# Kernel optimization log

Hardware: AMD Instinct MI355X
Metric: run time of the kernel (lower is better)

The kernel has to match this reference:

```python
import jax, jax.numpy as jnp
import numpy as np


def setup_inputs() -> dict:
    key = jax.random.key(0)
    k1, k2, k3, k4 = jax.random.split(key, 4)
    B, S, IN, OUT = 4, 2048, 4096, 4096
    x = jax.random.normal(k1, (B, S, IN), dtype=jnp.float32)
    # 4-bit signed range [-8, 7], stored widened (torch uses int8)
    weight_quantized = jax.random.randint(k2, (OUT, IN), -8, 8, dtype=jnp.int32)
    # per-output-row scale, positive and small (abs-max / 7 style)
    weight_scale = jax.random.uniform(k3, (OUT,), dtype=jnp.float32) * 0.01 + 1e-4
    bias = jax.random.normal(k4, (OUT,), dtype=jnp.float32) * 0.01
    return {"x": x, "weight_quantized": weight_quantized,
            "weight_scale": weight_scale, "bias": bias}


def reference(x, weight_quantized, weight_scale, bias):
    # dequantize: [OUT, IN] int -> fp32 scaled per output row
    w = weight_quantized.astype(jnp.float32) * weight_scale[:, None]
    # F.linear: x @ w.T + bias  -> [B, S, OUT]
    out = jnp.einsum('bsi,oi->bso', x, w) + bias
    return out
```

## Files before the change

kernel.cpp:

```cpp
#include <hip/hip_runtime.h>
#include <hip/hip_bf16.h>

typedef __bf16 bf16x4 __attribute__((ext_vector_type(4)));
typedef __bf16 bf16x8 __attribute__((ext_vector_type(8)));
typedef float  floatx4 __attribute__((ext_vector_type(4)));

#define AS1 __attribute__((address_space(1)))
#define AS3 __attribute__((address_space(3)))

#define BM2 256
#define BN2 256
#define BK2 64
#define HALF (128 * 64)
#define ABUF (2 * HALF)

#define BARRIER() asm volatile("s_barrier" ::: "memory")

__global__ __launch_bounds__(256)
void cvt_both8(const float* __restrict__ xin, const int* __restrict__ win,
               __bf16* __restrict__ xout, __bf16* __restrict__ wout,
               int nx8, int nw8)
{
    const int stride = gridDim.x * 256;
    const int total  = nx8 + nw8;
    for (int i = blockIdx.x * 256 + threadIdx.x; i < total; i += stride) {
        if (i < nx8) {
            const float4* p = reinterpret_cast<const float4*>(xin) + (size_t)i * 2;
            float4 a = p[0], b = p[1];
            bf16x8 h;
            h[0] = (__bf16)a.x; h[1] = (__bf16)a.y; h[2] = (__bf16)a.z; h[3] = (__bf16)a.w;
            h[4] = (__bf16)b.x; h[5] = (__bf16)b.y; h[6] = (__bf16)b.z; h[7] = (__bf16)b.w;
            reinterpret_cast<bf16x8*>(xout)[i] = h;
        } else {
            int j = i - nx8;
            const int4* p = reinterpret_cast<const int4*>(win) + (size_t)j * 2;
            int4 a = p[0], b = p[1];
            bf16x8 h;
            h[0] = (__bf16)(float)a.x; h[1] = (__bf16)(float)a.y;
            h[2] = (__bf16)(float)a.z; h[3] = (__bf16)(float)a.w;
            h[4] = (__bf16)(float)b.x; h[5] = (__bf16)(float)b.y;
            h[6] = (__bf16)(float)b.z; h[7] = (__bf16)(float)b.w;
            reinterpret_cast<bf16x8*>(wout)[j] = h;
        }
    }
}

template<int Q>
__device__ __forceinline__ void mfma16(floatx4 (&acc)[8][4],
                                       const bf16x8 (&af)[2][2],
                                       const bf16x8 (&bfr)[4][2])
{
#pragma unroll
    for (int h = 0; h < 2; ++h)
#pragma unroll
        for (int ii = 0; ii < 2; ++ii)
#pragma unroll
            for (int j = 0; j < 4; ++j)
                acc[2 * Q + ii][j] = __builtin_amdgcn_mfma_f32_16x16x32_bf16(
                    af[ii][h], bfr[j][h], acc[2 * Q + ii][j], 0, 0, 0);
}

__device__ __forceinline__ void read_afH(bf16x8 (&dst)[2][2], const __bf16* p,
                                         int rowBase, int lm, int kq, int sw)
{
#pragma unroll
    for (int ii = 0; ii < 2; ++ii)
#pragma unroll
        for (int h = 0; h < 2; ++h)
            dst[ii][h] = *reinterpret_cast<const bf16x8*>(
                &p[(rowBase + ii * 16 + lm) * 64 + ((kq + h * 4) ^ sw) * 8]);
}

__device__ __forceinline__ void read_bfH(bf16x8 (&dst)[4][2], const __bf16* p,
                                         int wnh, int lm, int kq, int sw)
{
#pragma unroll
    for (int j = 0; j < 4; ++j)
#pragma unroll
        for (int h = 0; h < 2; ++h)
            dst[j][h] = *reinterpret_cast<const bf16x8*>(
                &p[(wnh + j * 16 + lm) * 64 + ((kq + h * 4) ^ sw) * 8]);
}

__global__ __launch_bounds__(512)
void gemm_bf16_bt_8ph(const __bf16* __restrict__ A, const __bf16* __restrict__ B,
                      const float* __restrict__ scale, const float* __restrict__ bias,
                      float* __restrict__ Out, int M, int N, int K)
{
    __shared__ __bf16 sA[2 * ABUF];
    __shared__ __bf16 sB[2 * ABUF];

    const int tid  = threadIdx.x;
    const int wave = tid >> 6;
    const int lane = tid & 63;
    const int row0 = blockIdx.y * BM2;
    const int col0 = blockIdx.x * BN2;

    const int sRow = lane >> 3;
    const int gBlk = (lane & 7) ^ sRow;
    const size_t aBase = (size_t)(row0 + wave * 8 + sRow) * K + gBlk * 8;
    const size_t bBase = (size_t)(col0 + wave * 8 + sRow) * K + gBlk * 8;
    const int dOff = wave * 8 * 64;

#define STG_A(buf, h, sub, kt_) \
    __builtin_amdgcn_global_load_lds( \
        (const AS1 void*)(A + aBase + (size_t)((h) * 128 + (sub) * 64) * K + (size_t)(kt_) * BK2), \
        (AS3 void*)(sA + (buf) * ABUF + (h) * HALF + (sub) * 64 * 64 + dOff), 16, 0, 0)
#define STG_B(buf, h, sub, kt_) \
    __builtin_amdgcn_global_load_lds( \
        (const AS1 void*)(B + bBase + (size_t)((h) * 128 + (sub) * 64) * K + (size_t)(kt_) * BK2), \
        (AS3 void*)(sB + (buf) * ABUF + (h) * HALF + (sub) * 64 * 64 + dOff), 16, 0, 0)
#define STGH_A(buf, h, kt_) do { STG_A(buf, h, 0, kt_); STG_A(buf, h, 1, kt_); } while (0)
#define STGH_B(buf, h, kt_) do { STG_B(buf, h, 0, kt_); STG_B(buf, h, 1, kt_); } while (0)

    const int hA  = wave >> 2;
    const int hB  = (wave & 3) >> 1;
    const int wnh = (wave & 1) * 64;
    const int lm  = lane & 15;
    const int kq  = lane >> 4;
    const int sw  = lm & 7;

    const __bf16* aH[2] = { sA + hA * HALF, sA + ABUF + hA * HALF };
    const __bf16* bH[2] = { sB + hB * HALF, sB + ABUF + hB * HALF };

    floatx4 acc[8][4];
#pragma unroll
    for (int i = 0; i < 8; ++i)
#pragma unroll
        for (int j = 0; j < 4; ++j)
            acc[i][j] = (floatx4)0.0f;

    bf16x8 bfr[4][2];
    bf16x8 af[2][2];
    const int nt = K / BK2;

    STGH_B(0, 0, 0); STGH_B(0, 1, 0);
    STGH_A(0, 0, 0); STGH_A(0, 1, 0);
    STGH_B(1, 0, 1); STGH_B(1, 1, 1);
    asm volatile("s_waitcnt vmcnt(4)" ::: "memory");
    BARRIER();

#define PH(Q, c, DOB, STAGE, DOVM)                                             \
    do {                                                                       \
        if (DOB) read_bfH(bfr, bH[c], wnh, lm, kq, sw);                        \
        read_afH(af, aH[c], (Q) * 32, lm, kq, sw);                             \
        STAGE;                                                                 \
        BARRIER();                                                             \
        __builtin_amdgcn_sched_barrier(0);                                     \
        __builtin_amdgcn_s_setprio(1);                                         \
        mfma16<Q>(acc, af, bfr);                                               \
        __builtin_amdgcn_s_setprio(0);                                         \
        __builtin_amdgcn_sched_barrier(0);                                     \
        if (DOVM) asm volatile("s_waitcnt vmcnt(4)" ::: "memory");             \
        BARRIER();                                                             \
    } while (0)

    for (int it = 0; it < nt / 2; ++it) {
        const int kt = 2 * it;
        const int e1 = kt + 1;
        const int e2 = (kt + 2 < nt) ? kt + 2 : 0;
        const int e3 = (kt + 3 < nt) ? kt + 3 : 0;

        PH(0, 0, true,  STGH_A(1, 0, e1), false);
        PH(1, 0, false, STGH_A(1, 1, e1), false);
        PH(2, 0, false, STGH_B(0, 0, e2), false);
        PH(3, 0, false, STGH_B(0, 1, e2), true );
        PH(0, 1, true,  STGH_A(0, 0, e2), false);
        PH(1, 1, false, STGH_A(0, 1, e2), false);
        PH(2, 1, false, STGH_B(1, 0, e3), false);
        PH(3, 1, false, STGH_B(1, 1, e3), true );
    }
    asm volatile("s_waitcnt vmcnt(0)" ::: "memory");
#undef PH
#undef STGH_A
#undef STGH_B
#undef STG_A
#undef STG_B

    const int wm = hA * 128;
    const int wn = (wave & 3) * 64;
#pragma unroll
    for (int j = 0; j < 4; ++j) {
        int n = col0 + wn + j * 16 + lm;
        float sc = scale[n];
        float bi = bias[n];
#pragma unroll
        for (int i = 0; i < 8; ++i) {
#pragma unroll
            for (int r = 0; r < 4; ++r) {
                int m = row0 + wm + i * 16 + kq * 4 + r;
                Out[(size_t)m * N + n] = sc * acc[i][j][r] + bi;
            }
        }
    }
}

#define BM 128
#define BN 128

__global__ __launch_bounds__(256)
void fp4linear_gemm(const float* __restrict__ X, const int* __restrict__ W,
                    const float* __restrict__ scale, const float* __restrict__ bias,
                    float* __restrict__ Out, int M, int N, int K)
{
    __shared__ __bf16 sA[BM * 32];
    __shared__ __bf16 sB[BN * 32];

    const int tid  = threadIdx.x;
    const int row0 = blockIdx.y * BM;
    const int col0 = blockIdx.x * BN;
    const int wave = tid >> 6;
    const int lane = tid & 63;
    const int wm = (wave >> 1) * 64;
    const int wn = (wave & 1) * 64;
    const int lm = lane & 15;
    const int kq = lane >> 4;

    floatx4 acc[4][4];
#pragma unroll
    for (int i = 0; i < 4; ++i)
#pragma unroll
        for (int j = 0; j < 4; ++j)
            acc[i][j] = (floatx4)0.0f;

    for (int k0 = 0; k0 < K; k0 += 32) {
        float4 fa[4];
        int4   ib[4];
#pragma unroll
        for (int l = 0; l < 4; ++l) {
            int idx = tid + l * 256;
            int r = idx >> 3, c4 = idx & 7;
            fa[l] = *reinterpret_cast<const float4*>(
                        &X[(size_t)(row0 + r) * K + k0 + c4 * 4]);
        }
#pragma unroll
        for (int l = 0; l < 4; ++l) {
            int idx = tid + l * 256;
            int r = idx >> 3, c4 = idx & 7;
            ib[l] = *reinterpret_cast<const int4*>(
                        &W[(size_t)(col0 + r) * K + k0 + c4 * 4]);
        }
        __syncthreads();
#pragma unroll
        for (int l = 0; l < 4; ++l) {
            int idx = tid + l * 256;
            int r = idx >> 3, c4 = idx & 7;
            bf16x4 h;
            h[0] = (__bf16)fa[l].x; h[1] = (__bf16)fa[l].y;
            h[2] = (__bf16)fa[l].z; h[3] = (__bf16)fa[l].w;
            *reinterpret_cast<bf16x4*>(&sA[r * 32 + c4 * 4]) = h;
        }
#pragma unroll
        for (int l = 0; l < 4; ++l) {
            int idx = tid + l * 256;
            int r = idx >> 3, c4 = idx & 7;
            bf16x4 h;
            h[0] = (__bf16)(float)ib[l].x; h[1] = (__bf16)(float)ib[l].y;
            h[2] = (__bf16)(float)ib[l].z; h[3] = (__bf16)(float)ib[l].w;
            *reinterpret_cast<bf16x4*>(&sB[r * 32 + c4 * 4]) = h;
        }
        __syncthreads();

        bf16x8 af[4], bfr[4];
#pragma unroll
        for (int i = 0; i < 4; ++i)
            af[i] = *reinterpret_cast<const bf16x8*>(
                        &sA[(wm + i * 16 + lm) * 32 + kq * 8]);
#pragma unroll
        for (int j = 0; j < 4; ++j)
            bfr[j] = *reinterpret_cast<const bf16x8*>(
                        &sB[(wn + j * 16 + lm) * 32 + kq * 8]);
#pragma unroll
        for (int i = 0; i < 4; ++i)
#pragma unroll
            for (int j = 0; j < 4; ++j)
                acc[i][j] = __builtin_amdgcn_mfma_f32_16x16x32_bf16(
                                af[i], bfr[j], acc[i][j], 0, 0, 0);
    }

#pragma unroll
    for (int j = 0; j < 4; ++j) {
        int n = col0 + wn + j * 16 + lm;
        float sc = scale[n];
        float bi = bias[n];
#pragma unroll
        for (int i = 0; i < 4; ++i) {
#pragma unroll
            for (int r = 0; r < 4; ++r) {
                int m = row0 + wm + i * 16 + kq * 4 + r;
                Out[(size_t)m * N + n] = sc * acc[i][j][r] + bi;
            }
        }
    }
}

extern "C" void kernel_launch(void* const* d_in, const int* in_sizes, int n_in,
                              void* d_out, int out_size, void* d_ws, size_t ws_size,
                              hipStream_t stream) {
    const float* x     = (const float*)d_in[0];
    const int*   wq    = (const int*)d_in[1];
    const float* scale = (const float*)d_in[2];
    const float* bias  = (const float*)d_in[3];
    float* out = (float*)d_out;

    const int N = in_sizes[2];
    const int K = in_sizes[1] / N;
    const int M = in_sizes[0] / K;

    const size_t xElems = (size_t)M * K;
    const size_t wElems = (size_t)N * K;
    const size_t need   = (xElems + wElems) * sizeof(__bf16);

    const bool cvt_ok = (ws_size >= need) && (xElems % 8 == 0) && (wElems % 8 == 0);
    const int  nt     = K / BK2;
    const bool gemm_ok = (M % BM2 == 0) && (N % BN2 == 0) && (K % BK2 == 0) &&
                         (nt % 2 == 0) && (nt >= 4);

    if (cvt_ok && gemm_ok) {
        __bf16* xb = (__bf16*)d_ws;
        __bf16* wb = xb + xElems;
        int nx8 = (int)(xElems / 8);
        int nw8 = (int)(wElems / 8);
        int total = nx8 + nw8;
        int cvtBlocks = (total + 255) / 256;
        if (cvtBlocks > 2048) cvtBlocks = 2048;
        hipLaunchKernelGGL(cvt_both8, dim3(cvtBlocks), dim3(256), 0, stream,
                           x, wq, xb, wb, nx8, nw8);
        hipLaunchKernelGGL(gemm_bf16_bt_8ph, dim3(N / BN2, M / BM2), dim3(512),
                           0, stream, xb, wb, scale, bias, out, M, N, K);
        return;
    }

    hipLaunchKernelGGL(fp4linear_gemm, dim3(N / BN, M / BM), dim3(256), 0, stream,
                       x, wq, scale, bias, out, M, N, K);
}
```

Baseline: 508.5 us.

## Fuse fp32/int32-to-bf16 conversion into GEMM tile loading via register staging

Drops the separate conversion kernel that wrote bf16 copies of x and the weights to workspace. The GEMM now loads fp32 activations and int32 weights directly, converts them in registers and writes swizzled bf16 tiles to LDS, using a reworked phase pipeline that splits the B fragments into two halves. This removes the extra global write and re-read of the converted operands and one kernel launch. In exchange, each tile fetches twice the bytes from global memory, the operands are re-read and re-converted across the many output tiles, and the direct global-to-LDS async loads become register round-trips with more VGPR pressure.

After: 1.185 ms. 133% more time.

```diff
diff --git a/kernel.cpp b/kernel.cpp
--- a/kernel.cpp
+++ b/kernel.cpp
@@ -16,48 +16,25 @@
 
 #define BARRIER() asm volatile("s_barrier" ::: "memory")
 
-__global__ __launch_bounds__(256)
-void cvt_both8(const float* __restrict__ xin, const int* __restrict__ win,
-               __bf16* __restrict__ xout, __bf16* __restrict__ wout,
-               int nx8, int nw8)
-{
-    const int stride = gridDim.x * 256;
-    const int total  = nx8 + nw8;
-    for (int i = blockIdx.x * 256 + threadIdx.x; i < total; i += stride) {
-        if (i < nx8) {
-            const float4* p = reinterpret_cast<const float4*>(xin) + (size_t)i * 2;
-            float4 a = p[0], b = p[1];
-            bf16x8 h;
-            h[0] = (__bf16)a.x; h[1] = (__bf16)a.y; h[2] = (__bf16)a.z; h[3] = (__bf16)a.w;
-            h[4] = (__bf16)b.x; h[5] = (__bf16)b.y; h[6] = (__bf16)b.z; h[7] = (__bf16)b.w;
-            reinterpret_cast<bf16x8*>(xout)[i] = h;
-        } else {
-            int j = i - nx8;
-            const int4* p = reinterpret_cast<const int4*>(win) + (size_t)j * 2;
-            int4 a = p[0], b = p[1];
-            bf16x8 h;
-            h[0] = (__bf16)(float)a.x; h[1] = (__bf16)(float)a.y;
-            h[2] = (__bf16)(float)a.z; h[3] = (__bf16)(float)a.w;
-            h[4] = (__bf16)(float)b.x; h[5] = (__bf16)(float)b.y;
-            h[6] = (__bf16)(float)b.z; h[7] = (__bf16)(float)b.w;
-            reinterpret_cast<bf16x8*>(wout)[j] = h;
-        }
-    }
-}
-
 template<int Q>
-__device__ __forceinline__ void mfma16(floatx4 (&acc)[8][4],
-                                       const bf16x8 (&af)[2][2],
-                                       const bf16x8 (&bfr)[4][2])
+__device__ __forceinline__ void mfma16s(floatx4 (&acc)[8][4],
+                                        const bf16x8 (&af)[2][2],
+                                        const bf16x8 (&bfA)[2][2],
+                                        const bf16x8 (&bfB)[2][2])
 {
 #pragma unroll
     for (int h = 0; h < 2; ++h)
 #pragma unroll
-        for (int ii = 0; ii < 2; ++ii)
-#pragma unroll
-            for (int j = 0; j < 4; ++j)
+        for (int ii = 0; ii < 2; ++ii) {
+#pragma unroll
+            for (int j = 0; j < 2; ++j)
                 acc[2 * Q + ii][j] = __builtin_amdgcn_mfma_f32_16x16x32_bf16(
-                    af[ii][h], bfr[j][h], acc[2 * Q + ii][j], 0, 0, 0);
+                    af[ii][h], bfA[j][h], acc[2 * Q + ii][j], 0, 0, 0);
+#pragma unroll
+            for (int j = 0; j < 2; ++j)
+                acc[2 * Q + ii][2 + j] = __builtin_amdgcn_mfma_f32_16x16x32_bf16(
+                    af[ii][h], bfB[j][h], acc[2 * Q + ii][2 + j], 0, 0, 0);
+        }
 }
 
 __device__ __forceinline__ void read_afH(bf16x8 (&dst)[2][2], const __bf16* p,
@@ -68,24 +45,24 @@
 #pragma unroll
         for (int h = 0; h < 2; ++h)
             dst[ii][h] = *reinterpret_cast<const bf16x8*>(
-                &p[(rowBase + ii * 16 + lm) * 64 + ((kq + h * 4) ^ sw) * 8]);
-}
-
-__device__ __forceinline__ void read_bfH(bf16x8 (&dst)[4][2], const __bf16* p,
-                                         int wnh, int lm, int kq, int sw)
-{
-#pragma unroll
-    for (int j = 0; j < 4; ++j)
+                &p[(rowBase + ii * 16 + lm) * BK2 + ((kq + h * 4) ^ sw) * 8]);
+}
+
+__device__ __forceinline__ void read_bf2(bf16x8 (&dst)[2][2], const __bf16* p,
+                                         int rowBase, int lm, int kq, int sw)
+{
+#pragma unroll
+    for (int j = 0; j < 2; ++j)
 #pragma unroll
         for (int h = 0; h < 2; ++h)
             dst[j][h] = *reinterpret_cast<const bf16x8*>(
-                &p[(wnh + j * 16 + lm) * 64 + ((kq + h * 4) ^ sw) * 8]);
+                &p[(rowBase + j * 16 + lm) * BK2 + ((kq + h * 4) ^ sw) * 8]);
 }
 
 __global__ __launch_bounds__(512)
-void gemm_bf16_bt_8ph(const __bf16* __restrict__ A, const __bf16* __restrict__ B,
-                      const float* __restrict__ scale, const float* __restrict__ bias,
-                      float* __restrict__ Out, int M, int N, int K)
+void gemm_fused(const float* __restrict__ X, const int* __restrict__ W,
+                const float* __restrict__ scale, const float* __restrict__ bias,
+                float* __restrict__ Out, int M, int N, int K)
 {
     __shared__ __bf16 sA[2 * ABUF];
     __shared__ __bf16 sB[2 * ABUF];
@@ -96,22 +73,44 @@
     const int row0 = blockIdx.y * BM2;
     const int col0 = blockIdx.x * BN2;
 
-    const int sRow = lane >> 3;
-    const int gBlk = (lane & 7) ^ sRow;
-    const size_t aBase = (size_t)(row0 + wave * 8 + sRow) * K + gBlk * 8;
-    const size_t bBase = (size_t)(col0 + wave * 8 + sRow) * K + gBlk * 8;
-    const int dOff = wave * 8 * 64;
-
-#define STG_A(buf, h, sub, kt_) \
-    __builtin_amdgcn_global_load_lds( \
-        (const AS1 void*)(A + aBase + (size_t)((h) * 128 + (sub) * 64) * K + (size_t)(kt_) * BK2), \
-        (AS3 void*)(sA + (buf) * ABUF + (h) * HALF + (sub) * 64 * 64 + dOff), 16, 0, 0)
-#define STG_B(buf, h, sub, kt_) \
-    __builtin_amdgcn_global_load_lds( \
-        (const AS1 void*)(B + bBase + (size_t)((h) * 128 + (sub) * 64) * K + (size_t)(kt_) * BK2), \
-        (AS3 void*)(sB + (buf) * ABUF + (h) * HALF + (sub) * 64 * 64 + dOff), 16, 0, 0)
-#define STGH_A(buf, h, kt_) do { STG_A(buf, h, 0, kt_); STG_A(buf, h, 1, kt_); } while (0)
-#define STGH_B(buf, h, kt_) do { STG_B(buf, h, 0, kt_); STG_B(buf, h, 1, kt_); } while (0)
+    const float* Ab = X + (size_t)row0 * K;
+    const int*   Wb = W + (size_t)col0 * K;
+
+#define U_ROW(j) ((tid + (j) * 512) >> 4)
+#define U_CB(j)  ((tid + (j) * 512) & 15)
+
+#define LD_CHUNK(set, SRC, h, kt_)                                             \
+    do { _Pragma("unroll") for (int j = 0; j < 4; ++j) {                       \
+        set[j] = *reinterpret_cast<const int4*>(                               \
+            (SRC) + (size_t)((h) * 128 + U_ROW(j)) * K                         \
+                  + (size_t)(kt_) * 64 + U_CB(j) * 4);                         \
+    } } while (0)
+
+#define LDS_BYTE(j, base2)                                                     \
+    ((base2) + U_ROW(j) * 128 + (((U_CB(j) >> 1) ^ (U_ROW(j) & 7)) * 16)       \
+             + (U_CB(j) & 1) * 8)
+
+#define WR_CHUNK_A(set, buf, h)                                                \
+    do { _Pragma("unroll") for (int j = 0; j < 4; ++j) {                       \
+        bf16x4 hv;                                                             \
+        hv[0] = (__bf16)__int_as_float(set[j].x);                              \
+        hv[1] = (__bf16)__int_as_float(set[j].y);                              \
+        hv[2] = (__bf16)__int_as_float(set[j].z);                              \
+        hv[3] = (__bf16)__int_as_float(set[j].w);                              \
+        *reinterpret_cast<bf16x4*>((char*)sA +                                 \
+            LDS_BYTE(j, ((buf) * ABUF + (h) * HALF) * 2)) = hv;                \
+    } } while (0)
+
+#define WR_CHUNK_B(set, buf, h)                                                \
+    do { _Pragma("unroll") for (int j = 0; j < 4; ++j) {                       \
+        bf16x4 hv;                                                             \
+        hv[0] = (__bf16)(float)set[j].x;                                       \
+        hv[1] = (__bf16)(float)set[j].y;                                       \
+        hv[2] = (__bf16)(float)set[j].z;                                       \
+        hv[3] = (__bf16)(float)set[j].w;                                       \
+        *reinterpret_cast<bf16x4*>((char*)sB +                                 \
+            LDS_BYTE(j, ((buf) * ABUF + (h) * HALF) * 2)) = hv;                \
+    } } while (0)
 
     const int hA  = wave >> 2;
     const int hB  = (wave & 3) >> 1;
@@ -130,52 +129,64 @@
         for (int j = 0; j < 4; ++j)
             acc[i][j] = (floatx4)0.0f;
 
-    bf16x8 bfr[4][2];
-    bf16x8 af[2][2];
+    bf16x8 bfA[2][2], bfB[2][2], af[2][2];
+    int4 s0[4], s1[4];
     const int nt = K / BK2;
 
-    STGH_B(0, 0, 0); STGH_B(0, 1, 0);
-    STGH_A(0, 0, 0); STGH_A(0, 1, 0);
-    STGH_B(1, 0, 1); STGH_B(1, 1, 1);
-    asm volatile("s_waitcnt vmcnt(4)" ::: "memory");
+    LD_CHUNK(s0, Ab, 0, 0); WR_CHUNK_A(s0, 0, 0);
+    LD_CHUNK(s0, Ab, 1, 0); WR_CHUNK_A(s0, 0, 1);
+    LD_CHUNK(s0, Wb, 0, 0); WR_CHUNK_B(s0, 0, 0);
+    LD_CHUNK(s0, Wb, 1, 0); WR_CHUNK_B(s0, 0, 1);
+    LD_CHUNK(s0, Wb, 0, 1); WR_CHUNK_B(s0, 1, 0);
+    LD_CHUNK(s1, Wb, 1, 1);
+    asm volatile("s_waitcnt lgkmcnt(0)" ::: "memory");
     BARRIER();
-
-#define PH(Q, c, DOB, STAGE, DOVM)                                             \
+    read_bf2(bfA, bH[0], wnh, lm, kq, sw);
+
+#define PHASE(Q, c, HEADX, ISSUE, POSTX, WRX)                                  \
     do {                                                                       \
-        if (DOB) read_bfH(bfr, bH[c], wnh, lm, kq, sw);                        \
+        HEADX;                                                                 \
         read_afH(af, aH[c], (Q) * 32, lm, kq, sw);                             \
-        STAGE;                                                                 \
+        ISSUE;                                                                 \
         BARRIER();                                                             \
         __builtin_amdgcn_sched_barrier(0);                                     \
         __builtin_amdgcn_s_setprio(1);                                         \
-        mfma16<Q>(acc, af, bfr);                                               \
+        mfma16s<Q>(acc, af, bfA, bfB);                                         \
         __builtin_amdgcn_s_setprio(0);                                         \
         __builtin_amdgcn_sched_barrier(0);                                     \
-        if (DOVM) asm volatile("s_waitcnt vmcnt(4)" ::: "memory");             \
+        POSTX;                                                                 \
+        WRX;                                                                   \
+        asm volatile("s_waitcnt lgkmcnt(0)" ::: "memory");                     \
         BARRIER();                                                             \
     } while (0)
+
+#define TILE(c, e1, e2)                                                        \
+    PHASE(0, c, read_bf2(bfB, bH[c], wnh + 32, lm, kq, sw),                    \
+          LD_CHUNK(s0, Ab, 0, e1), (void)0, WR_CHUNK_B(s1, (c) ^ 1, 1));       \
+    PHASE(1, c, (void)0, LD_CHUNK(s1, Ab, 1, e1), (void)0,                     \
+          WR_CHUNK_A(s0, (c) ^ 1, 0));                                         \
+    PHASE(2, c, (void)0, LD_CHUNK(s0, Wb, 0, e2), (void)0,                     \
+          WR_CHUNK_A(s1, (c) ^ 1, 1));                                         \
+    PHASE(3, c, (void)0, LD_CHUNK(s1, Wb, 1, e2),                              \
+          read_bf2(bfA, bH[(c) ^ 1], wnh, lm, kq, sw), WR_CHUNK_B(s0, (c), 0));
 
     for (int it = 0; it < nt / 2; ++it) {
         const int kt = 2 * it;
         const int e1 = kt + 1;
         const int e2 = (kt + 2 < nt) ? kt + 2 : 0;
-        const int e3 = (kt + 3 < nt) ? kt + 3 : 0;
-
-        PH(0, 0, true,  STGH_A(1, 0, e1), false);
-        PH(1, 0, false, STGH_A(1, 1, e1), false);
-        PH(2, 0, false, STGH_B(0, 0, e2), false);
-        PH(3, 0, false, STGH_B(0, 1, e2), true );
-        PH(0, 1, true,  STGH_A(0, 0, e2), false);
-        PH(1, 1, false, STGH_A(0, 1, e2), false);
-        PH(2, 1, false, STGH_B(1, 0, e3), false);
-        PH(3, 1, false, STGH_B(1, 1, e3), true );
-    }
-    asm volatile("s_waitcnt vmcnt(0)" ::: "memory");
-#undef PH
-#undef STGH_A
-#undef STGH_B
-#undef STG_A
-#undef STG_B
+        const int f2 = (kt + 3 < nt) ? kt + 3 : 0;
+        TILE(0, e1, e2)
+        TILE(1, e2, f2)
+    }
+    asm volatile("s_waitcnt vmcnt(0) lgkmcnt(0)" ::: "memory");
+#undef TILE
+#undef PHASE
+#undef WR_CHUNK_A
+#undef WR_CHUNK_B
+#undef LDS_BYTE
+#undef LD_CHUNK
+#undef U_ROW
+#undef U_CB
 
     const int wm = hA * 128;
     const int wn = (wave & 3) * 64;
@@ -307,27 +318,13 @@
     const int K = in_sizes[1] / N;
     const int M = in_sizes[0] / K;
 
-    const size_t xElems = (size_t)M * K;
-    const size_t wElems = (size_t)N * K;
-    const size_t need   = (xElems + wElems) * sizeof(__bf16);
-
-    const bool cvt_ok = (ws_size >= need) && (xElems % 8 == 0) && (wElems % 8 == 0);
-    const int  nt     = K / BK2;
+    const int  nt      = K / BK2;
     const bool gemm_ok = (M % BM2 == 0) && (N % BN2 == 0) && (K % BK2 == 0) &&
                          (nt % 2 == 0) && (nt >= 4);
 
-    if (cvt_ok && gemm_ok) {
-        __bf16* xb = (__bf16*)d_ws;
-        __bf16* wb = xb + xElems;
-        int nx8 = (int)(xElems / 8);
-        int nw8 = (int)(wElems / 8);
-        int total = nx8 + nw8;
-        int cvtBlocks = (total + 255) / 256;
-        if (cvtBlocks > 2048) cvtBlocks = 2048;
-        hipLaunchKernelGGL(cvt_both8, dim3(cvtBlocks), dim3(256), 0, stream,
-                           x, wq, xb, wb, nx8, nw8);
-        hipLaunchKernelGGL(gemm_bf16_bt_8ph, dim3(N / BN2, M / BM2), dim3(512),
-                           0, stream, xb, wb, scale, bias, out, M, N, K);
+    if (gemm_ok) {
+        hipLaunchKernelGGL(gemm_fused, dim3(N / BN2, M / BM2), dim3(512),
+                           0, stream, x, wq, scale, bias, out, M, N, K);
         return;
     }
 
```
